# Kernel optimization log

Hardware: AMD Instinct MI355X
Metric: run time of the kernel (lower is better)

Reference implementation:

```python
import jax, jax.numpy as jnp
import numpy as np

B, D, H, T, F = 2, 256, 8, 128, 64
C = H * F          # channels = 512
TE = 512           # time_embed_dim


def setup_inputs() -> dict:
    key = jax.random.key(0)
    ks = jax.random.split(key, 9)
    pd = jax.random.randint(ks[2], (B, T, T), 0, 2 * T - 1, dtype=jnp.int32) - (T - 1)
    s = 0.02
    return {
        "qk": jax.random.normal(ks[0], (B, D, H, T, F), jnp.float32),
        "temb": jax.random.normal(ks[1], (B, T, TE), jnp.float32),
        "pairwise_distances": pd,
        "w_dist": jax.random.normal(ks[3], (3, C), jnp.float32) * s,
        "b_dist": jax.random.normal(ks[4], (C,), jnp.float32) * s,
        "w_time": jax.random.normal(ks[5], (TE, C), jnp.float32) * s,
        "b_time": jax.random.normal(ks[6], (C,), jnp.float32) * s,
        "w_out": jax.random.normal(ks[7], (C, C), jnp.float32) * s,
        "b_out": jax.random.normal(ks[8], (C,), jnp.float32) * s,
    }


def _rpe_net(temb, pd, w_dist, b_dist, w_time, b_time, w_out, b_out):
    d = pd.astype(jnp.float32)
    # (B, T, S, 3): log(1+d+), log(1+d-), indicator(d==0)
    dist_embs = jnp.stack(
        [jnp.log1p(jnp.maximum(d, 0.0)),
         jnp.log1p(jnp.maximum(-d, 0.0)),
         (pd == 0).astype(jnp.float32)],
        axis=-1,
    )
    emb = (temb @ w_time + b_time)[:, :, None, :] + dist_embs @ w_dist + b_dist  # (B,T,S,C)
    R = jax.nn.silu(emb) @ w_out + b_out  # (B,T,S,C)
    return R.reshape(*pd.shape, H, F)     # (B,T,S,H,F)


def reference(qk, temb, pairwise_distances, w_dist, b_dist, w_time, b_time, w_out, b_out):
    R = _rpe_net(temb, pairwise_distances, w_dist, b_dist, w_time, b_time, w_out, b_out)
    # forward_qk: contract head_dim f for every (t, s) pair
    return jnp.einsum('bdhtf,btshf->bdhts', qk, R)
```

## Files before the change

kernel.cpp:

```cpp
#include <hip/hip_runtime.h>
#include <hip/hip_bf16.h>

#define B_  2
#define D_  256
#define H_  8
#define T_  128
#define S_  128
#define F_  64
#define C_  512
#define TE_ 512

typedef _Float16 f16x8 __attribute__((ext_vector_type(8)));
typedef _Float16 f16x4 __attribute__((ext_vector_type(4)));
typedef float    f32x4 __attribute__((ext_vector_type(4)));

#define AS1 __attribute__((address_space(1)))
#define AS3 __attribute__((address_space(3)))

__global__ __launch_bounds__(128) void k_time_proj(
    const float* __restrict__ temb, const float* __restrict__ w_time,
    const float* __restrict__ b_time, const float* __restrict__ b_dist,
    float* __restrict__ tp)
{
    int row = blockIdx.x;
    int tid = threadIdx.x;
    __shared__ float te[TE_];
    for (int i = tid; i < TE_; i += 128)
        te[i] = temb[(size_t)row * TE_ + i];
    __syncthreads();
    int c0 = tid * 4;
    float4 b0 = *(const float4*)&b_time[c0];
    float4 b1 = *(const float4*)&b_dist[c0];
    float ax0 = 0.f, ay0 = 0.f, az0 = 0.f, aw0 = 0.f;
    float ax1 = 0.f, ay1 = 0.f, az1 = 0.f, aw1 = 0.f;
#pragma unroll 4
    for (int e = 0; e < TE_; e += 2) {
        float s0 = te[e], s1 = te[e + 1];
        float4 w0 = *(const float4*)&w_time[(size_t)e * C_ + c0];
        float4 w1 = *(const float4*)&w_time[(size_t)(e + 1) * C_ + c0];
        ax0 += s0 * w0.x; ay0 += s0 * w0.y; az0 += s0 * w0.z; aw0 += s0 * w0.w;
        ax1 += s1 * w1.x; ay1 += s1 * w1.y; az1 += s1 * w1.z; aw1 += s1 * w1.w;
    }
    float4 r;
    r.x = b0.x + b1.x + ax0 + ax1;
    r.y = b0.y + b1.y + ay0 + ay1;
    r.z = b0.z + b1.z + az0 + az1;
    r.w = b0.w + b1.w + aw0 + aw1;
    *(float4*)&tp[(size_t)row * C_ + c0] = r;
}

__global__ __launch_bounds__(128) void k_embed_silu(
    const float* __restrict__ tp, const int* __restrict__ pd,
    const float* __restrict__ w_dist, _Float16* __restrict__ A)
{
    int row = blockIdx.x;
    int bt  = row >> 7;
    int d   = pd[row];
    float f0 = log1pf(fmaxf((float)d, 0.f));
    float f1 = log1pf(fmaxf((float)(-d), 0.f));
    float f2 = (d == 0) ? 1.f : 0.f;
    int c0 = threadIdx.x * 4;
    float4 t4 = *(const float4*)&tp[(size_t)bt * C_ + c0];
    float4 w0 = *(const float4*)&w_dist[c0];
    float4 w1 = *(const float4*)&w_dist[C_ + c0];
    float4 w2 = *(const float4*)&w_dist[2 * C_ + c0];
    float e0 = t4.x + f0 * w0.x + f1 * w1.x + f2 * w2.x;
    float e1 = t4.y + f0 * w0.y + f1 * w1.y + f2 * w2.y;
    float e2 = t4.z + f0 * w0.z + f1 * w1.z + f2 * w2.z;
    float e3 = t4.w + f0 * w0.w + f1 * w1.w + f2 * w2.w;
    f16x4 v;
    v.x = (_Float16)(e0 / (1.f + expf(-e0)));
    v.y = (_Float16)(e1 / (1.f + expf(-e1)));
    v.z = (_Float16)(e2 / (1.f + expf(-e2)));
    v.w = (_Float16)(e3 / (1.f + expf(-e3)));
    *(f16x4*)&A[(size_t)row * C_ + c0] = v;
}

__global__ __launch_bounds__(512) void k_wt(
    const float* __restrict__ w_out, _Float16* __restrict__ Wt)
{
    int n = blockIdx.x;
    int k = threadIdx.x;
    Wt[(size_t)n * C_ + k] = (_Float16)w_out[(size_t)k * C_ + n];
}

__global__ __launch_bounds__(256) void k_gemm_R(
    const _Float16* __restrict__ A, const _Float16* __restrict__ Wt,
    const float* __restrict__ b_out, _Float16* __restrict__ R)
{
    const int K = 512, N = 512;
    __shared__ _Float16 As[128][64];
    __shared__ _Float16 Bs[128][64];
    int bm = blockIdx.x, bn = blockIdx.y;
    int tid = threadIdx.x;
    int wave = tid >> 6, lane = tid & 63;
    int wm = (wave >> 1) * 64, wn = (wave & 1) * 64;
    int mrow = lane & 15, kq = (lane >> 4) * 8;
    int grow = lane >> 3;
    int gcol = (lane & 7) * 8;
    const size_t arow0 = (size_t)bm * 128;
    const size_t brow0 = (size_t)bn * 128;
    f32x4 acc[4][4] = {};
    for (int k0 = 0; k0 < K; k0 += 64) {
#pragma unroll
        for (int p = 0; p < 4; ++p) {
            int rb = (p * 4 + wave) * 8;
            __builtin_amdgcn_global_load_lds(
                (const AS1 void*)(const void*)&A[(arow0 + rb + grow) * K + k0 + gcol],
                (AS3 void*)(void*)&As[rb][0], 16, 0, 0);
            __builtin_amdgcn_global_load_lds(
                (const AS1 void*)(const void*)&Wt[(brow0 + rb + grow) * K + k0 + gcol],
                (AS3 void*)(void*)&Bs[rb][0], 16, 0, 0);
        }
        __syncthreads();
#pragma unroll
        for (int ks = 0; ks < 64; ks += 32) {
            f16x8 af[4], bfr[4];
#pragma unroll
            for (int i = 0; i < 4; ++i) af[i]  = *(const f16x8*)&As[wm + i * 16 + mrow][ks + kq];
#pragma unroll
            for (int j = 0; j < 4; ++j) bfr[j] = *(const f16x8*)&Bs[wn + j * 16 + mrow][ks + kq];
#pragma unroll
            for (int i = 0; i < 4; ++i)
#pragma unroll
                for (int j = 0; j < 4; ++j)
                    acc[i][j] = __builtin_amdgcn_mfma_f32_16x16x32_f16(af[i], bfr[j], acc[i][j], 0, 0, 0);
        }
        __syncthreads();
    }
    int col = lane & 15, rb = (lane >> 4) * 4;
#pragma unroll
    for (int j = 0; j < 4; ++j) {
        int n = bn * 128 + wn + j * 16 + col;
        float bo = b_out[n];
#pragma unroll
        for (int i = 0; i < 4; ++i)
#pragma unroll
            for (int r = 0; r < 4; ++r) {
                size_t m = arow0 + wm + i * 16 + rb + r;
                R[m * N + n] = (_Float16)(acc[i][j][r] + bo);
            }
    }
}

__global__ __launch_bounds__(256) void k_einsum(
    const float* __restrict__ qk, const _Float16* __restrict__ R,
    float* __restrict__ out)
{
    int bht  = blockIdx.x;
    int dblk = blockIdx.y;
    int t = bht & 127;
    int h = (bht >> 7) & 7;
    int b = bht >> 10;
    int tid = threadIdx.x;
    int wave = tid >> 6, lane = tid & 63;
    int wm = (wave >> 1) * 64, wn = (wave & 1) * 64;
    int mrow = lane & 15, kq = (lane >> 4) * 8;

    const size_t qstr  = (size_t)(H_ * T_ * F_);
    const size_t qbase = (size_t)b * (D_ * H_ * T_ * F_) + (size_t)h * (T_ * F_)
                       + (size_t)t * F_ + (size_t)dblk * 128 * qstr;
    const size_t rbase = ((size_t)(b * T_ + t) * S_) * C_ + h * 64;

    f32x4 acc[4][4] = {};
#pragma unroll
    for (int ks = 0; ks < 64; ks += 32) {
        f16x8 bf[4], aq[4];
#pragma unroll
        for (int j = 0; j < 4; ++j)
            bf[j] = *(const f16x8*)&R[rbase + (size_t)(wn + j * 16 + mrow) * C_ + ks + kq];
#pragma unroll
        for (int i = 0; i < 4; ++i) {
            const float* qp = &qk[qbase + (size_t)(wm + i * 16 + mrow) * qstr + ks + kq];
            float4 u = *(const float4*)qp;
            float4 v = *(const float4*)(qp + 4);
            f16x8 a;
            a[0] = (_Float16)u.x; a[1] = (_Float16)u.y;
            a[2] = (_Float16)u.z; a[3] = (_Float16)u.w;
            a[4] = (_Float16)v.x; a[5] = (_Float16)v.y;
            a[6] = (_Float16)v.z; a[7] = (_Float16)v.w;
            aq[i] = a;
        }
#pragma unroll
        for (int j = 0; j < 4; ++j)
#pragma unroll
            for (int i = 0; i < 4; ++i)
                acc[j][i] = __builtin_amdgcn_mfma_f32_16x16x32_f16(bf[j], aq[i], acc[j][i], 0, 0, 0);
    }

    const size_t ostr  = (size_t)(H_ * T_ * S_);
    const size_t obase = (size_t)b * (D_ * H_ * T_ * S_) + (size_t)h * (T_ * S_)
                       + (size_t)t * S_ + (size_t)dblk * 128 * ostr;
    int dcol = lane & 15, sb = (lane >> 4) * 4;
#pragma unroll
    for (int i = 0; i < 4; ++i) {
        size_t orow = obase + (size_t)(wm + i * 16 + dcol) * ostr + wn + sb;
#pragma unroll
        for (int j = 0; j < 4; ++j)
            *(f32x4*)&out[orow + j * 16] = acc[j][i];
    }
}

extern "C" void kernel_launch(void* const* d_in, const int* in_sizes, int n_in,
                              void* d_out, int out_size, void* d_ws, size_t ws_size,
                              hipStream_t stream) {
    (void)in_sizes; (void)n_in; (void)out_size; (void)ws_size;
    const float* qk     = (const float*)d_in[0];
    const float* temb   = (const float*)d_in[1];
    const int*   pd     = (const int*)d_in[2];
    const float* w_dist = (const float*)d_in[3];
    const float* b_dist = (const float*)d_in[4];
    const float* w_time = (const float*)d_in[5];
    const float* b_time = (const float*)d_in[6];
    const float* w_out  = (const float*)d_in[7];
    const float* b_out  = (const float*)d_in[8];
    float* out = (float*)d_out;

    char* ws = (char*)d_ws;
    float*     tp = (float*)ws;
    _Float16*  Wt = (_Float16*)(ws + 512 * 1024);
    _Float16*  A  = (_Float16*)(ws + 1024 * 1024);
    _Float16*  R  = (_Float16*)(ws + 1024 * 1024 + 33554432);

    k_time_proj<<<dim3(B_ * T_), dim3(128), 0, stream>>>(temb, w_time, b_time, b_dist, tp);
    k_wt<<<dim3(C_), dim3(C_), 0, stream>>>(w_out, Wt);
    k_embed_silu<<<dim3(B_ * T_ * S_), dim3(128), 0, stream>>>(tp, pd, w_dist, A);
    k_gemm_R<<<dim3(256, 4), dim3(256), 0, stream>>>(A, Wt, b_out, R);
    k_einsum<<<dim3(B_ * H_ * T_, 2), dim3(256), 0, stream>>>(qk, R, out);
}
```

Measured before the change: 512.4 us.

## Fuse R GEMM with einsum, keeping R tile in swizzled LDS

Merges the R-producing GEMM and the einsum into one kernel. Each block computes the R tile for one (b,t) over half the channels (four heads), stores it as fp16 in XOR-swizzled shared memory, then runs the per-head einsum MFMAs directly from LDS. This removes the global write and re-read of the 32 MB R intermediate and one kernel launch. In exchange it uses much more LDS per block (about 112 KB), which lowers occupancy, and serializes the four heads' qk loads and output stores within each block.

Result: no change. 520.3 us (+1.5%).

```diff
diff --git a/kernel.cpp b/kernel.cpp
--- a/kernel.cpp
+++ b/kernel.cpp
@@ -69,10 +69,10 @@
     float e2 = t4.z + f0 * w0.z + f1 * w1.z + f2 * w2.z;
     float e3 = t4.w + f0 * w0.w + f1 * w1.w + f2 * w2.w;
     f16x4 v;
-    v.x = (_Float16)(e0 / (1.f + expf(-e0)));
-    v.y = (_Float16)(e1 / (1.f + expf(-e1)));
-    v.z = (_Float16)(e2 / (1.f + expf(-e2)));
-    v.w = (_Float16)(e3 / (1.f + expf(-e3)));
+    v[0] = (_Float16)(e0 / (1.f + expf(-e0)));
+    v[1] = (_Float16)(e1 / (1.f + expf(-e1)));
+    v[2] = (_Float16)(e2 / (1.f + expf(-e2)));
+    v[3] = (_Float16)(e3 / (1.f + expf(-e3)));
     *(f16x4*)&A[(size_t)row * C_ + c0] = v;
 }
 
@@ -84,120 +84,124 @@
     Wt[(size_t)n * C_ + k] = (_Float16)w_out[(size_t)k * C_ + n];
 }
 
-__global__ __launch_bounds__(256) void k_gemm_R(
-    const _Float16* __restrict__ A, const _Float16* __restrict__ Wt,
-    const float* __restrict__ b_out, _Float16* __restrict__ R)
-{
-    const int K = 512, N = 512;
-    __shared__ _Float16 As[128][64];
-    __shared__ _Float16 Bs[128][64];
-    int bm = blockIdx.x, bn = blockIdx.y;
-    int tid = threadIdx.x;
+__global__ __launch_bounds__(512) void k_fused(
+    const float* __restrict__ qk, const _Float16* __restrict__ A,
+    const _Float16* __restrict__ Wt, const float* __restrict__ b_out,
+    float* __restrict__ out)
+{
+    __shared__ alignas(16) _Float16 Rs[128][256];
+    __shared__ alignas(16) _Float16 As[128][64];
+    __shared__ alignas(16) _Float16 Wts[256][64];
+
+    int bt = blockIdx.x >> 1;
+    int hg = blockIdx.x & 1;
+    int b  = bt >> 7, t = bt & 127;
+    int tid  = threadIdx.x;
     int wave = tid >> 6, lane = tid & 63;
-    int wm = (wave >> 1) * 64, wn = (wave & 1) * 64;
     int mrow = lane & 15, kq = (lane >> 4) * 8;
-    int grow = lane >> 3;
-    int gcol = (lane & 7) * 8;
-    const size_t arow0 = (size_t)bm * 128;
-    const size_t brow0 = (size_t)bn * 128;
+    int grow = lane >> 3, gcol = (lane & 7) * 8;
+
+    int wm1 = (wave & 1) * 64;
+    int wn1 = (wave >> 1) * 64;
+    const size_t arow0 = (size_t)bt * 128;
     f32x4 acc[4][4] = {};
-    for (int k0 = 0; k0 < K; k0 += 64) {
-#pragma unroll
-        for (int p = 0; p < 4; ++p) {
-            int rb = (p * 4 + wave) * 8;
+    for (int k0 = 0; k0 < 512; k0 += 64) {
+#pragma unroll
+        for (int q = 0; q < 2; ++q) {
+            int ch = wave * 2 + q;
             __builtin_amdgcn_global_load_lds(
-                (const AS1 void*)(const void*)&A[(arow0 + rb + grow) * K + k0 + gcol],
-                (AS3 void*)(void*)&As[rb][0], 16, 0, 0);
+                (const AS1 void*)(const void*)&A[(arow0 + ch * 8 + grow) * 512 + k0 + gcol],
+                (AS3 void*)(void*)&As[ch * 8][0], 16, 0, 0);
+        }
+#pragma unroll
+        for (int q = 0; q < 4; ++q) {
+            int ch = wave * 4 + q;
             __builtin_amdgcn_global_load_lds(
-                (const AS1 void*)(const void*)&Wt[(brow0 + rb + grow) * K + k0 + gcol],
-                (AS3 void*)(void*)&Bs[rb][0], 16, 0, 0);
+                (const AS1 void*)(const void*)&Wt[(size_t)(hg * 256 + ch * 8 + grow) * 512 + k0 + gcol],
+                (AS3 void*)(void*)&Wts[ch * 8][0], 16, 0, 0);
         }
         __syncthreads();
 #pragma unroll
         for (int ks = 0; ks < 64; ks += 32) {
-            f16x8 af[4], bfr[4];
-#pragma unroll
-            for (int i = 0; i < 4; ++i) af[i]  = *(const f16x8*)&As[wm + i * 16 + mrow][ks + kq];
-#pragma unroll
-            for (int j = 0; j < 4; ++j) bfr[j] = *(const f16x8*)&Bs[wn + j * 16 + mrow][ks + kq];
-#pragma unroll
-            for (int i = 0; i < 4; ++i)
-#pragma unroll
-                for (int j = 0; j < 4; ++j)
-                    acc[i][j] = __builtin_amdgcn_mfma_f32_16x16x32_f16(af[i], bfr[j], acc[i][j], 0, 0, 0);
+            f16x8 af[4], wtf[4];
+#pragma unroll
+            for (int i = 0; i < 4; ++i) af[i]  = *(const f16x8*)&As[wm1 + i * 16 + mrow][ks + kq];
+#pragma unroll
+            for (int j = 0; j < 4; ++j) wtf[j] = *(const f16x8*)&Wts[wn1 + j * 16 + mrow][ks + kq];
+#pragma unroll
+            for (int j = 0; j < 4; ++j)
+#pragma unroll
+                for (int i = 0; i < 4; ++i)
+                    acc[j][i] = __builtin_amdgcn_mfma_f32_16x16x32_f16(wtf[j], af[i], acc[j][i], 0, 0, 0);
         }
         __syncthreads();
     }
-    int col = lane & 15, rb = (lane >> 4) * 4;
-#pragma unroll
-    for (int j = 0; j < 4; ++j) {
-        int n = bn * 128 + wn + j * 16 + col;
-        float bo = b_out[n];
-#pragma unroll
-        for (int i = 0; i < 4; ++i)
-#pragma unroll
-            for (int r = 0; r < 4; ++r) {
-                size_t m = arow0 + wm + i * 16 + rb + r;
-                R[m * N + n] = (_Float16)(acc[i][j][r] + bo);
+    char* rsb = (char*)&Rs[0][0];
+    {
+        int cg = (lane >> 4) * 4;
+#pragma unroll
+        for (int j = 0; j < 4; ++j) {
+            int c = wn1 + j * 16 + cg;
+            float4 bo = *(const float4*)&b_out[hg * 256 + c];
+#pragma unroll
+            for (int i = 0; i < 4; ++i) {
+                int s = wm1 + i * 16 + mrow;
+                f16x4 hv;
+                hv[0] = (_Float16)(acc[j][i][0] + bo.x);
+                hv[1] = (_Float16)(acc[j][i][1] + bo.y);
+                hv[2] = (_Float16)(acc[j][i][2] + bo.z);
+                hv[3] = (_Float16)(acc[j][i][3] + bo.w);
+                *(f16x4*)(rsb + ((((s << 8) + c) << 1) ^ ((s & 1) << 6))) = hv;
             }
-    }
-}
-
-__global__ __launch_bounds__(256) void k_einsum(
-    const float* __restrict__ qk, const _Float16* __restrict__ R,
-    float* __restrict__ out)
-{
-    int bht  = blockIdx.x;
-    int dblk = blockIdx.y;
-    int t = bht & 127;
-    int h = (bht >> 7) & 7;
-    int b = bht >> 10;
-    int tid = threadIdx.x;
-    int wave = tid >> 6, lane = tid & 63;
-    int wm = (wave >> 1) * 64, wn = (wave & 1) * 64;
-    int mrow = lane & 15, kq = (lane >> 4) * 8;
-
-    const size_t qstr  = (size_t)(H_ * T_ * F_);
-    const size_t qbase = (size_t)b * (D_ * H_ * T_ * F_) + (size_t)h * (T_ * F_)
-                       + (size_t)t * F_ + (size_t)dblk * 128 * qstr;
-    const size_t rbase = ((size_t)(b * T_ + t) * S_) * C_ + h * 64;
-
-    f32x4 acc[4][4] = {};
-#pragma unroll
-    for (int ks = 0; ks < 64; ks += 32) {
-        f16x8 bf[4], aq[4];
-#pragma unroll
-        for (int j = 0; j < 4; ++j)
-            bf[j] = *(const f16x8*)&R[rbase + (size_t)(wn + j * 16 + mrow) * C_ + ks + kq];
+        }
+    }
+    __syncthreads();
+
+    int wm2 = (wave >> 1) * 64;
+    int wn2 = (wave & 1) * 64;
+    const size_t qstr = (size_t)(H_ * T_ * F_);
+    const size_t ostr = (size_t)(H_ * T_ * S_);
+    int dcol = lane & 15, sb = (lane >> 4) * 4;
+    for (int hp = 0; hp < 4; ++hp) {
+        int h = hg * 4 + hp;
+        const size_t qbase = (size_t)b * (D_ * H_ * T_ * F_) + (size_t)h * (T_ * F_)
+                           + (size_t)t * F_;
+        f32x4 acc2[4][4] = {};
+#pragma unroll
+        for (int ks = 0; ks < 64; ks += 32) {
+            f16x8 rf[4], qf[4];
+#pragma unroll
+            for (int j = 0; j < 4; ++j) {
+                int s = wn2 + j * 16 + mrow;
+                rf[j] = *(const f16x8*)(rsb + ((((s << 8) + hp * 64 + ks + kq) << 1) ^ ((s & 1) << 6)));
+            }
+#pragma unroll
+            for (int i = 0; i < 4; ++i) {
+                const float* qp = &qk[qbase + (size_t)(wm2 + i * 16 + mrow) * qstr + ks + kq];
+                float4 u = *(const float4*)qp;
+                float4 v = *(const float4*)(qp + 4);
+                f16x8 a;
+                a[0] = (_Float16)u.x; a[1] = (_Float16)u.y;
+                a[2] = (_Float16)u.z; a[3] = (_Float16)u.w;
+                a[4] = (_Float16)v.x; a[5] = (_Float16)v.y;
+                a[6] = (_Float16)v.z; a[7] = (_Float16)v.w;
+                qf[i] = a;
+            }
+#pragma unroll
+            for (int j = 0; j < 4; ++j)
+#pragma unroll
+                for (int i = 0; i < 4; ++i)
+                    acc2[j][i] = __builtin_amdgcn_mfma_f32_16x16x32_f16(rf[j], qf[i], acc2[j][i], 0, 0, 0);
+        }
+        const size_t obase = (size_t)b * (D_ * H_ * T_ * S_) + (size_t)h * (T_ * S_)
+                           + (size_t)t * S_;
 #pragma unroll
         for (int i = 0; i < 4; ++i) {
-            const float* qp = &qk[qbase + (size_t)(wm + i * 16 + mrow) * qstr + ks + kq];
-            float4 u = *(const float4*)qp;
-            float4 v = *(const float4*)(qp + 4);
-            f16x8 a;
-            a[0] = (_Float16)u.x; a[1] = (_Float16)u.y;
-            a[2] = (_Float16)u.z; a[3] = (_Float16)u.w;
-            a[4] = (_Float16)v.x; a[5] = (_Float16)v.y;
-            a[6] = (_Float16)v.z; a[7] = (_Float16)v.w;
-            aq[i] = a;
-        }
-#pragma unroll
-        for (int j = 0; j < 4; ++j)
-#pragma unroll
-            for (int i = 0; i < 4; ++i)
-                acc[j][i] = __builtin_amdgcn_mfma_f32_16x16x32_f16(bf[j], aq[i], acc[j][i], 0, 0, 0);
-    }
-
-    const size_t ostr  = (size_t)(H_ * T_ * S_);
-    const size_t obase = (size_t)b * (D_ * H_ * T_ * S_) + (size_t)h * (T_ * S_)
-                       + (size_t)t * S_ + (size_t)dblk * 128 * ostr;
-    int dcol = lane & 15, sb = (lane >> 4) * 4;
-#pragma unroll
-    for (int i = 0; i < 4; ++i) {
-        size_t orow = obase + (size_t)(wm + i * 16 + dcol) * ostr + wn + sb;
-#pragma unroll
-        for (int j = 0; j < 4; ++j)
-            *(f32x4*)&out[orow + j * 16] = acc[j][i];
+            size_t orow = obase + (size_t)(wm2 + i * 16 + dcol) * ostr;
+#pragma unroll
+            for (int j = 0; j < 4; ++j)
+                *(f32x4*)&out[orow + wn2 + j * 16 + sb] = acc2[j][i];
+        }
     }
 }
 
@@ -220,11 +224,9 @@
     float*     tp = (float*)ws;
     _Float16*  Wt = (_Float16*)(ws + 512 * 1024);
     _Float16*  A  = (_Float16*)(ws + 1024 * 1024);
-    _Float16*  R  = (_Float16*)(ws + 1024 * 1024 + 33554432);
 
     k_time_proj<<<dim3(B_ * T_), dim3(128), 0, stream>>>(temb, w_time, b_time, b_dist, tp);
     k_wt<<<dim3(C_), dim3(C_), 0, stream>>>(w_out, Wt);
     k_embed_silu<<<dim3(B_ * T_ * S_), dim3(128), 0, stream>>>(tp, pd, w_dist, A);
-    k_gemm_R<<<dim3(256, 4), dim3(256), 0, stream>>>(A, Wt, b_out, R);
-    k_einsum<<<dim3(B_ * H_ * T_, 2), dim3(256), 0, stream>>>(qk, R, out);
-}
+    k_fused<<<dim3(B_ * T_ * 2), dim3(512), 0, stream>>>(qk, A, Wt, b_out, out);
+}
```
